# Performance work log

Hardware: AMD Instinct MI355X
Metric: run time of the kernel (lower is better)

## Reference

```python
import jax, jax.numpy as jnp
import numpy as np

WS = 7          # window size
NH = 16         # n_heads
DIM = 512
HEAD_DIM = DIM // NH
SCALE = HEAD_DIM ** -0.5


def _rel_pos_index(ws):
    coords = np.stack(np.meshgrid(np.arange(ws), np.arange(ws), indexing='ij'))  # [2,ws,ws]
    coords = coords.reshape(2, -1)                                               # [2,N]
    rel = coords[:, :, None] - coords[:, None, :]                                # [2,N,N]
    idx = (rel[0] + ws - 1) * (2 * ws - 1) + (rel[1] + ws - 1)                   # [N,N]
    return jnp.asarray(idx, dtype=jnp.int32)


def _window_partition(x, ws):
    B, H, W, C = x.shape
    x = x.reshape(B, H // ws, ws, W // ws, ws, C)
    x = x.transpose(0, 1, 3, 2, 4, 5)
    return x.reshape(-1, ws * ws, C)  # [B*nW, N, C]


def setup_inputs() -> dict:
    key = jax.random.key(0)
    k1, k2, k3 = jax.random.split(key, 3)
    qkv = jax.random.normal(k1, (3, 32, 56, 56, DIM), dtype=jnp.float32)
    mask = jax.random.normal(k2, (64, WS * WS, WS * WS), dtype=jnp.float32)
    bias_table = jax.random.normal(k3, ((2 * WS - 1) ** 2, NH), dtype=jnp.float32) * 0.02
    return {"qkv": qkv, "mask": mask, "bias_table": bias_table}


def reference(qkv, mask, bias_table):
    q, k, v = qkv[0], qkv[1], qkv[2]
    B, H, W, C = q.shape
    N = WS * WS
    # window partition + split heads -> [BS, NH, N, HEAD_DIM]
    def prep(x):
        x = _window_partition(x, WS)                       # [BS, N, C]
        BS = x.shape[0]
        return x.reshape(BS, N, NH, HEAD_DIM).transpose(0, 2, 1, 3)
    q, k, v = prep(q), prep(k), prep(v)
    BS = q.shape[0]

    attn = jnp.einsum('bhnd,bhmd->bhnm', q, k) * SCALE      # [BS, NH, N, N]

    idx = _rel_pos_index(WS)                                # [N, N] static
    rel_bias = bias_table[idx]                              # [N, N, NH]
    attn = attn + rel_bias.transpose(2, 0, 1)[None]         # [BS, NH, N, N]

    nW = mask.shape[0]
    attn = attn.reshape(BS // nW, nW, NH, N, N) + mask[None, :, None]
    attn = attn.reshape(BS, NH, N, N)

    attn = jax.nn.softmax(attn, axis=-1)
    x = jnp.einsum('bhnm,bhmd->bhnd', attn, v)              # [BS, NH, N, HEAD_DIM]
    return x.transpose(0, 2, 1, 3).reshape(BS, N, C)
```

## Files before the change

kernel.cpp:

```cpp
#include <hip/hip_runtime.h>

#define NTOK 49
#define NH 16
#define DIM 512
#define HD 32
#define HPB 4
#define SCALE 0.17677669529663687f

typedef __attribute__((ext_vector_type(8))) short short8;
typedef __attribute__((ext_vector_type(16))) float f32x16;

struct __attribute__((packed, aligned(4))) f4u { float x, y, z, w; };

__device__ __forceinline__ unsigned short f2b(float x) {
    union { float f; unsigned u; } v; v.f = x;
    unsigned u = v.u;
    u += 0x7fffu + ((u >> 16) & 1u);
    return (unsigned short)(u >> 16);
}

__device__ __forceinline__ float b2f(unsigned short b) {
    union { unsigned u; float f; } v; v.u = ((unsigned)b) << 16;
    return v.f;
}

__device__ __forceinline__ unsigned long long pack4(float4 v) {
    unsigned lo = (unsigned)f2b(v.x) | ((unsigned)f2b(v.y) << 16);
    unsigned hi = (unsigned)f2b(v.z) | ((unsigned)f2b(v.w) << 16);
    return (unsigned long long)lo | ((unsigned long long)hi << 32);
}

__device__ __forceinline__ short8 pack8s(float4 a, float4 b, float sc) {
    short8 r;
    r[0] = (short)f2b(a.x * sc); r[1] = (short)f2b(a.y * sc);
    r[2] = (short)f2b(a.z * sc); r[3] = (short)f2b(a.w * sc);
    r[4] = (short)f2b(b.x * sc); r[5] = (short)f2b(b.y * sc);
    r[6] = (short)f2b(b.z * sc); r[7] = (short)f2b(b.w * sc);
    return r;
}

__global__ __launch_bounds__(256, 4) void winattn_mfma(
    const float* __restrict__ qkv,
    const float* __restrict__ mask,
    const float* __restrict__ bias_table,
    float* __restrict__ out)
{
    __shared__ __align__(16) unsigned short Vr[HPB][64][32];
    __shared__ __align__(8)  unsigned short maskw[HPB][2404];
    __shared__ float biasw[HPB][176];
    __shared__ float invl[HPB][64];

    const int bx   = blockIdx.x;
    const int win  = bx >> 2;
    const int hg   = bx & 3;
    const int tid  = threadIdx.x;
    const int wave = tid >> 6;
    const int lane = tid & 63;
    const int ln   = lane & 31;
    const int h    = lane >> 5;
    const int head = hg * HPB + wave;

    const int b  = win >> 6;
    const int w  = win & 63;
    const int wr = w >> 3, wc = w & 7;

    const size_t plane = (size_t)32 * 56 * 56 * 512;
    const size_t wbase = (((size_t)(b * 56 + wr * 7)) * 56 + wc * 7) * 512 + head * HD;

    const int t0 = ln;
    const int t1 = (32 + ln <= 48) ? (32 + ln) : 48;
    float4 qv[2][4], kv[2][4];
    #pragma unroll
    for (int tt = 0; tt < 2; ++tt) {
        const int t  = tt ? t1 : t0;
        const int i  = t / 7, j = t - i * 7;
        const float* qp = qkv + wbase + (size_t)(i * 56 + j) * 512 + h * 8;
        const float* kp = qp + plane;
        qv[tt][0] = *(const float4*)(qp);
        qv[tt][1] = *(const float4*)(qp + 4);
        qv[tt][2] = *(const float4*)(qp + 16);
        qv[tt][3] = *(const float4*)(qp + 20);
        kv[tt][0] = *(const float4*)(kp);
        kv[tt][1] = *(const float4*)(kp + 4);
        kv[tt][2] = *(const float4*)(kp + 16);
        kv[tt][3] = *(const float4*)(kp + 20);
    }

    #pragma unroll
    for (int e = 0; e < 8; ++e) {
        const int idx = e * 64 + lane;
        const int t   = idx >> 3;
        const int d4  = idx & 7;
        unsigned long long vz = 0;
        if (t < NTOK) {
            const int i = t / 7, j = t - i * 7;
            vz = pack4(*(const float4*)(qkv + 2 * plane + wbase
                                        + (size_t)(i * 56 + j) * 512 + d4 * 4));
        }
        *(unsigned long long*)&Vr[wave][t][d4 * 4] = vz;
    }

    const float* mrow = mask + (size_t)w * 2401;
    for (int e = lane; e < 600; e += 64) {
        f4u mv = *(const f4u*)(mrow + 4 * e);
        unsigned long long pk =
              (unsigned long long)f2b(mv.x)
            | ((unsigned long long)f2b(mv.y) << 16)
            | ((unsigned long long)f2b(mv.z) << 32)
            | ((unsigned long long)f2b(mv.w) << 48);
        *(unsigned long long*)&maskw[wave][4 * e] = pk;
    }
    if (lane == 0) maskw[wave][2400] = f2b(mrow[2400]);

    for (int r = lane; r < 169; r += 64)
        biasw[wave][r] = bias_table[r * NH + head];

    short8 qfr[2][2], kfr[2][2];
    #pragma unroll
    for (int tt = 0; tt < 2; ++tt) {
        qfr[tt][0] = pack8s(qv[tt][0], qv[tt][1], SCALE);
        qfr[tt][1] = pack8s(qv[tt][2], qv[tt][3], SCALE);
        kfr[tt][0] = pack8s(kv[tt][0], kv[tt][1], 1.0f);
        kfr[tt][1] = pack8s(kv[tt][2], kv[tt][3], 1.0f);
    }

    f32x16 zer;
    #pragma unroll
    for (int i = 0; i < 16; ++i) zer[i] = 0.f;
    f32x16 acc[2][2];
    acc[0][0] = zer; acc[0][1] = zer; acc[1][0] = zer; acc[1][1] = zer;
    #pragma unroll
    for (int ks = 0; ks < 2; ++ks) {
        acc[0][0] = __builtin_amdgcn_mfma_f32_32x32x16_bf16(kfr[0][ks], qfr[0][ks], acc[0][0], 0, 0, 0);
        acc[0][1] = __builtin_amdgcn_mfma_f32_32x32x16_bf16(kfr[0][ks], qfr[1][ks], acc[0][1], 0, 0, 0);
        acc[1][0] = __builtin_amdgcn_mfma_f32_32x32x16_bf16(kfr[1][ks], qfr[0][ks], acc[1][0], 0, 0, 0);
        acc[1][1] = __builtin_amdgcn_mfma_f32_32x32x16_bf16(kfr[1][ks], qfr[1][ks], acc[1][1], 0, 0, 0);
    }

    unsigned wpk[2][2][8];
    #pragma unroll
    for (int nt = 0; nt < 2; ++nt) {
        const int n  = 32 * nt + ln;
        const int nc = n < NTOK ? n : NTOK - 1;
        const int i_n = nc / 7;
        const int tn  = nc + 6 * i_n + 84;
        float pl[2][16];
        float mx = -3.0e38f;
        #pragma unroll
        for (int mt = 0; mt < 2; ++mt) {
            #pragma unroll
            for (int r = 0; r < 16; ++r) {
                const int mb  = 32 * mt + (r & 3) + 8 * (r >> 2);
                const int m0  = mb, m1 = mb + 4;
                const int mc0 = m0 < NTOK ? m0 : NTOK - 1;
                const int mc1 = m1 < NTOK ? m1 : NTOK - 1;
                const int tm0 = mc0 + 6 * (mc0 / 7);
                const int tm1 = mc1 + 6 * (mc1 / 7);
                const int mc  = h ? mc1 : mc0;
                const int tm  = h ? tm1 : tm0;
                float s = acc[mt][nt][r] + biasw[wave][tn - tm]
                        + b2f(maskw[wave][nc * NTOK + mc]);
                const bool dead = h ? (m1 >= NTOK) : (m0 >= NTOK);
                s = dead ? -3.0e38f : s;
                pl[mt][r] = s;
                mx = fmaxf(mx, s);
            }
        }
        mx = fmaxf(mx, __shfl_xor(mx, 32));
        float sum = 0.f;
        #pragma unroll
        for (int mt = 0; mt < 2; ++mt) {
            #pragma unroll
            for (int g = 0; g < 8; ++g) {
                const int ia = (g < 4) ? g : g + 4;
                const float e0 = __expf(pl[mt][ia] - mx);
                const float e1 = __expf(pl[mt][ia + 4] - mx);
                sum += e0 + e1;
                wpk[nt][mt][g] = (unsigned)f2b(e0) | ((unsigned)f2b(e1) << 16);
            }
        }
        sum += __shfl_xor(sum, 32);
        if (h == 0 && n < NTOK)
            invl[wave][n] = 1.0f / sum;
    }

    f32x16 oacc[2];
    oacc[0] = zer; oacc[1] = zer;
    #pragma unroll
    for (int ksv = 0; ksv < 4; ++ksv) {
        short8 vf;
        #pragma unroll
        for (int j = 0; j < 8; ++j)
            vf[j] = (short)Vr[wave][16 * ksv + 8 * h + j][ln];
        const int mt = ksv >> 1;
        #pragma unroll
        for (int nt = 0; nt < 2; ++nt) {
            unsigned short alo[4], ahi[4];
            #pragma unroll
            for (int jj = 0; jj < 4; ++jj) {
                const unsigned W = wpk[nt][mt][(ksv & 1) * 4 + jj];
                const unsigned U = (unsigned)__shfl_xor((int)W, 32);
                alo[jj] = h ? (unsigned short)(U >> 16) : (unsigned short)(W & 0xffffu);
                ahi[jj] = h ? (unsigned short)(W >> 16) : (unsigned short)(U & 0xffffu);
            }
            short8 af;
            af[0] = (short)alo[0]; af[1] = (short)alo[1];
            af[2] = (short)alo[2]; af[3] = (short)alo[3];
            af[4] = (short)ahi[0]; af[5] = (short)ahi[1];
            af[6] = (short)ahi[2]; af[7] = (short)ahi[3];
            oacc[nt] = __builtin_amdgcn_mfma_f32_32x32x16_bf16(af, vf, oacc[nt], 0, 0, 0);
        }
    }

    const size_t obase = ((size_t)win * NTOK) * DIM + head * HD + ln;
    #pragma unroll
    for (int nt = 0; nt < 2; ++nt) {
        #pragma unroll
        for (int r = 0; r < 16; ++r) {
            const int nb = 32 * nt + (r & 3) + 8 * (r >> 2);
            const int n  = h ? nb + 4 : nb;
            if (n < NTOK)
                out[obase + (size_t)n * DIM] = oacc[nt][r] * invl[wave][n];
        }
    }
}

extern "C" void kernel_launch(void* const* d_in, const int* in_sizes, int n_in,
                              void* d_out, int out_size, void* d_ws, size_t ws_size,
                              hipStream_t stream) {
    const float* qkv        = (const float*)d_in[0];
    const float* mask       = (const float*)d_in[1];
    const float* bias_table = (const float*)d_in[2];
    float* out = (float*)d_out;

    const int nblocks = 2048 * (NH / HPB);
    winattn_mfma<<<nblocks, 256, 0, stream>>>(qkv, mask, bias_table, out);
}
```

Baseline: 197.4 us.

## Pre-expand bias per head, seed MFMA accumulators with mask+bias, load V directly

Adds a small pre-kernel that expands the relative-position bias table into a dense per-head 49x49 workspace. The main kernel drops all shared-memory staging of V, mask and bias. It loads mask plus bias straight from global memory into the QK MFMA accumulators and gathers V per lane into registers as bf16 fragments. This removes the LDS fill and bf16 mask conversion and the per-element index arithmetic in softmax. In exchange it issues more scattered global loads, uses more registers (occupancy hint lowered to 3), and adds a second launch.

```diff
diff --git a/kernel.cpp b/kernel.cpp
--- a/kernel.cpp
+++ b/kernel.cpp
@@ -4,30 +4,17 @@
 #define NH 16
 #define DIM 512
 #define HD 32
-#define HPB 4
 #define SCALE 0.17677669529663687f
+#define NEGINF -3.0e38f
 
 typedef __attribute__((ext_vector_type(8))) short short8;
 typedef __attribute__((ext_vector_type(16))) float f32x16;
-
-struct __attribute__((packed, aligned(4))) f4u { float x, y, z, w; };
 
 __device__ __forceinline__ unsigned short f2b(float x) {
     union { float f; unsigned u; } v; v.f = x;
     unsigned u = v.u;
     u += 0x7fffu + ((u >> 16) & 1u);
     return (unsigned short)(u >> 16);
-}
-
-__device__ __forceinline__ float b2f(unsigned short b) {
-    union { unsigned u; float f; } v; v.u = ((unsigned)b) << 16;
-    return v.f;
-}
-
-__device__ __forceinline__ unsigned long long pack4(float4 v) {
-    unsigned lo = (unsigned)f2b(v.x) | ((unsigned)f2b(v.y) << 16);
-    unsigned hi = (unsigned)f2b(v.z) | ((unsigned)f2b(v.w) << 16);
-    return (unsigned long long)lo | ((unsigned long long)hi << 32);
 }
 
 __device__ __forceinline__ short8 pack8s(float4 a, float4 b, float sc) {
@@ -39,16 +26,25 @@
     return r;
 }
 
-__global__ __launch_bounds__(256, 4) void winattn_mfma(
+__global__ __launch_bounds__(256) void bias_expand_kernel(
+    const float* __restrict__ bt, float* __restrict__ bexp)
+{
+    const int e = blockIdx.x * 256 + threadIdx.x;
+    if (e >= NH * NTOK * NTOK) return;
+    const int head = e / (NTOK * NTOK);
+    const int rem  = e % (NTOK * NTOK);
+    const int n = rem / NTOK, m = rem % NTOK;
+    const int rel = (n / 7 - m / 7 + 6) * 13 + (n % 7 - m % 7 + 6);
+    bexp[e] = bt[rel * NH + head];
+}
+
+__global__ __launch_bounds__(256, 3) void winattn_mfma(
     const float* __restrict__ qkv,
     const float* __restrict__ mask,
-    const float* __restrict__ bias_table,
+    const float* __restrict__ bexp,
     float* __restrict__ out)
 {
-    __shared__ __align__(16) unsigned short Vr[HPB][64][32];
-    __shared__ __align__(8)  unsigned short maskw[HPB][2404];
-    __shared__ float biasw[HPB][176];
-    __shared__ float invl[HPB][64];
+    __shared__ float invl[4][64];
 
     const int bx   = blockIdx.x;
     const int win  = bx >> 2;
@@ -58,7 +54,7 @@
     const int lane = tid & 63;
     const int ln   = lane & 31;
     const int h    = lane >> 5;
-    const int head = hg * HPB + wave;
+    const int head = hg * 4 + wave;
 
     const int b  = win >> 6;
     const int w  = win & 63;
@@ -86,34 +82,35 @@
         kv[tt][3] = *(const float4*)(kp + 20);
     }
 
-    #pragma unroll
-    for (int e = 0; e < 8; ++e) {
-        const int idx = e * 64 + lane;
-        const int t   = idx >> 3;
-        const int d4  = idx & 7;
-        unsigned long long vz = 0;
-        if (t < NTOK) {
-            const int i = t / 7, j = t - i * 7;
-            vz = pack4(*(const float4*)(qkv + 2 * plane + wbase
-                                        + (size_t)(i * 56 + j) * 512 + d4 * 4));
-        }
-        *(unsigned long long*)&Vr[wave][t][d4 * 4] = vz;
-    }
-
-    const float* mrow = mask + (size_t)w * 2401;
-    for (int e = lane; e < 600; e += 64) {
-        f4u mv = *(const f4u*)(mrow + 4 * e);
-        unsigned long long pk =
-              (unsigned long long)f2b(mv.x)
-            | ((unsigned long long)f2b(mv.y) << 16)
-            | ((unsigned long long)f2b(mv.z) << 32)
-            | ((unsigned long long)f2b(mv.w) << 48);
-        *(unsigned long long*)&maskw[wave][4 * e] = pk;
-    }
-    if (lane == 0) maskw[wave][2400] = f2b(mrow[2400]);
-
-    for (int r = lane; r < 169; r += 64)
-        biasw[wave][r] = bias_table[r * NH + head];
+    const float* mrow = mask + (size_t)w * (NTOK * NTOK);
+    const float* brow = bexp + (size_t)head * (NTOK * NTOK);
+    f32x16 acc[2][2];
+    #pragma unroll
+    for (int nt = 0; nt < 2; ++nt) {
+        const int n  = 32 * nt + ln;
+        const int nc = n < NTOK ? n : NTOK - 1;
+        const float* mh = mrow + nc * NTOK + h * 4;
+        const float* bh = brow + nc * NTOK + h * 4;
+        const float* m0 = mrow + nc * NTOK;
+        const float* b0 = brow + nc * NTOK;
+        #pragma unroll
+        for (int r = 0; r < 16; ++r) {
+            const int mb = (r & 3) + 8 * (r >> 2);
+            acc[0][nt][r] = mh[mb] + bh[mb];
+        }
+        #pragma unroll
+        for (int r = 0; r < 16; ++r) {
+            const int mb = 32 + (r & 3) + 8 * (r >> 2);
+            if (mb <= 43) {
+                acc[1][nt][r] = mh[mb] + bh[mb];
+            } else if (mb == 48) {
+                const float v = m0[48] + b0[48];
+                acc[1][nt][r] = h ? NEGINF : v;
+            } else {
+                acc[1][nt][r] = NEGINF;
+            }
+        }
+    }
 
     short8 qfr[2][2], kfr[2][2];
     #pragma unroll
@@ -124,11 +121,6 @@
         kfr[tt][1] = pack8s(kv[tt][2], kv[tt][3], 1.0f);
     }
 
-    f32x16 zer;
-    #pragma unroll
-    for (int i = 0; i < 16; ++i) zer[i] = 0.f;
-    f32x16 acc[2][2];
-    acc[0][0] = zer; acc[0][1] = zer; acc[1][0] = zer; acc[1][1] = zer;
     #pragma unroll
     for (int ks = 0; ks < 2; ++ks) {
         acc[0][0] = __builtin_amdgcn_mfma_f32_32x32x16_bf16(kfr[0][ks], qfr[0][ks], acc[0][0], 0, 0, 0);
@@ -137,35 +129,37 @@
         acc[1][1] = __builtin_amdgcn_mfma_f32_32x32x16_bf16(kfr[1][ks], qfr[1][ks], acc[1][1], 0, 0, 0);
     }
 
+    const float* vwin = qkv + 2 * plane + wbase;
+    short8 vfr[4];
+    #pragma unroll
+    for (int ksv = 0; ksv < 4; ++ksv) {
+        float vt[8];
+        #pragma unroll
+        for (int j = 0; j < 8; ++j) {
+            const int ta = 16 * ksv + j;
+            const int tb = 16 * ksv + 8 + j;
+            const int tac = ta < NTOK ? ta : NTOK - 1;
+            const int tbc = tb < NTOK ? tb : NTOK - 1;
+            const int offa = ((tac / 7) * 56 + tac % 7) * 512;
+            const int offb = ((tbc / 7) * 56 + tbc % 7) * 512;
+            vt[j] = vwin[(h ? offb : offa) + ln];
+        }
+        short8 vf;
+        #pragma unroll
+        for (int j = 0; j < 8; ++j) vf[j] = (short)f2b(vt[j]);
+        vfr[ksv] = vf;
+    }
+
     unsigned wpk[2][2][8];
     #pragma unroll
     for (int nt = 0; nt < 2; ++nt) {
-        const int n  = 32 * nt + ln;
-        const int nc = n < NTOK ? n : NTOK - 1;
-        const int i_n = nc / 7;
-        const int tn  = nc + 6 * i_n + 84;
-        float pl[2][16];
-        float mx = -3.0e38f;
-        #pragma unroll
-        for (int mt = 0; mt < 2; ++mt) {
+        const int n = 32 * nt + ln;
+        float mx = NEGINF;
+        #pragma unroll
+        for (int mt = 0; mt < 2; ++mt)
             #pragma unroll
-            for (int r = 0; r < 16; ++r) {
-                const int mb  = 32 * mt + (r & 3) + 8 * (r >> 2);
-                const int m0  = mb, m1 = mb + 4;
-                const int mc0 = m0 < NTOK ? m0 : NTOK - 1;
-                const int mc1 = m1 < NTOK ? m1 : NTOK - 1;
-                const int tm0 = mc0 + 6 * (mc0 / 7);
-                const int tm1 = mc1 + 6 * (mc1 / 7);
-                const int mc  = h ? mc1 : mc0;
-                const int tm  = h ? tm1 : tm0;
-                float s = acc[mt][nt][r] + biasw[wave][tn - tm]
-                        + b2f(maskw[wave][nc * NTOK + mc]);
-                const bool dead = h ? (m1 >= NTOK) : (m0 >= NTOK);
-                s = dead ? -3.0e38f : s;
-                pl[mt][r] = s;
-                mx = fmaxf(mx, s);
-            }
-        }
+            for (int r = 0; r < 16; ++r)
+                mx = fmaxf(mx, acc[mt][nt][r]);
         mx = fmaxf(mx, __shfl_xor(mx, 32));
         float sum = 0.f;
         #pragma unroll
@@ -173,8 +167,8 @@
             #pragma unroll
             for (int g = 0; g < 8; ++g) {
                 const int ia = (g < 4) ? g : g + 4;
-                const float e0 = __expf(pl[mt][ia] - mx);
-                const float e1 = __expf(pl[mt][ia + 4] - mx);
+                const float e0 = __expf(acc[mt][nt][ia] - mx);
+                const float e1 = __expf(acc[mt][nt][ia + 4] - mx);
                 sum += e0 + e1;
                 wpk[nt][mt][g] = (unsigned)f2b(e0) | ((unsigned)f2b(e1) << 16);
             }
@@ -185,13 +179,11 @@
     }
 
     f32x16 oacc[2];
-    oacc[0] = zer; oacc[1] = zer;
+    #pragma unroll
+    for (int i = 0; i < 16; ++i) { oacc[0][i] = 0.f; oacc[1][i] = 0.f; }
     #pragma unroll
     for (int ksv = 0; ksv < 4; ++ksv) {
-        short8 vf;
-        #pragma unroll
-        for (int j = 0; j < 8; ++j)
-            vf[j] = (short)Vr[wave][16 * ksv + 8 * h + j][ln];
+        const short8 vf = vfr[ksv];
         const int mt = ksv >> 1;
         #pragma unroll
         for (int nt = 0; nt < 2; ++nt) {
@@ -231,8 +223,9 @@
     const float* qkv        = (const float*)d_in[0];
     const float* mask       = (const float*)d_in[1];
     const float* bias_table = (const float*)d_in[2];
-    float* out = (float*)d_out;
-
-    const int nblocks = 2048 * (NH / HPB);
-    winattn_mfma<<<nblocks, 256, 0, stream>>>(qkv, mask, bias_table, out);
-}
+    float* out  = (float*)d_out;
+    float* bexp = (float*)d_ws;
+
+    bias_expand_kernel<<<(NH * NTOK * NTOK + 255) / 256, 256, 0, stream>>>(bias_table, bexp);
+    winattn_mfma<<<2048 * 4, 256, 0, stream>>>(qkv, mask, bexp, out);
+}
```

Measured after the change: 243.1 us. 1.23x slower.

## Share a precomputed mask-plus-bias tile per block and drop the softmax max pass

Applied to the files above, without the earlier changes.

A small pre-kernel expands the relative-position bias table into a dense per-head 49x49 fp32 bias in workspace. Blocks are remapped so one block handles a single (window, head) pair and its four waves cover four batch images. Those waves can then share one fp32 shared-memory tile of mask plus bias, instead of each wave loading its own bf16 mask copy and bias slice. The softmax no longer computes or subtracts a row max and instead exponentiates the logits directly. This cuts shared and L2 traffic and ALU work, but it adds a second launch and a __syncthreads. It also gives up overflow protection on large logits.

```diff
diff --git a/kernel.cpp b/kernel.cpp
--- a/kernel.cpp
+++ b/kernel.cpp
@@ -4,24 +4,17 @@
 #define NH 16
 #define DIM 512
 #define HD 32
-#define HPB 4
 #define SCALE 0.17677669529663687f
+#define NEGINF -3.0e38f
 
 typedef __attribute__((ext_vector_type(8))) short short8;
 typedef __attribute__((ext_vector_type(16))) float f32x16;
-
-struct __attribute__((packed, aligned(4))) f4u { float x, y, z, w; };
 
 __device__ __forceinline__ unsigned short f2b(float x) {
     union { float f; unsigned u; } v; v.f = x;
     unsigned u = v.u;
     u += 0x7fffu + ((u >> 16) & 1u);
     return (unsigned short)(u >> 16);
-}
-
-__device__ __forceinline__ float b2f(unsigned short b) {
-    union { unsigned u; float f; } v; v.u = ((unsigned)b) << 16;
-    return v.f;
 }
 
 __device__ __forceinline__ unsigned long long pack4(float4 v) {
@@ -39,33 +32,55 @@
     return r;
 }
 
+__global__ __launch_bounds__(256) void bias_expand_kernel(
+    const float* __restrict__ bt, float* __restrict__ bexp)
+{
+    const int e = blockIdx.x * 256 + threadIdx.x;
+    if (e >= NH * NTOK * NTOK) return;
+    const int head = e / (NTOK * NTOK);
+    const int rem  = e % (NTOK * NTOK);
+    const int n = rem / NTOK, m = rem % NTOK;
+    const int rel = (n / 7 - m / 7 + 6) * 13 + (n % 7 - m % 7 + 6);
+    bexp[e] = bt[rel * NH + head];
+}
+
 __global__ __launch_bounds__(256, 4) void winattn_mfma(
     const float* __restrict__ qkv,
     const float* __restrict__ mask,
-    const float* __restrict__ bias_table,
+    const float* __restrict__ bexp,
     float* __restrict__ out)
 {
-    __shared__ __align__(16) unsigned short Vr[HPB][64][32];
-    __shared__ __align__(8)  unsigned short maskw[HPB][2404];
-    __shared__ float biasw[HPB][176];
-    __shared__ float invl[HPB][64];
+    __shared__ float comb[NTOK][66];
+    __shared__ __align__(16) unsigned short Vr[4][64][32];
+    __shared__ float invl[4][64];
 
     const int bx   = blockIdx.x;
-    const int win  = bx >> 2;
-    const int hg   = bx & 3;
+    const int head = bx & 15;
+    const int w    = (bx >> 4) & 63;
+    const int bg   = bx >> 10;
     const int tid  = threadIdx.x;
     const int wave = tid >> 6;
     const int lane = tid & 63;
     const int ln   = lane & 31;
     const int h    = lane >> 5;
-    const int head = hg * HPB + wave;
-
-    const int b  = win >> 6;
-    const int w  = win & 63;
-    const int wr = w >> 3, wc = w & 7;
+    const int b    = bg * 4 + wave;
+    const int win  = b * 64 + w;
+    const int wr   = w >> 3, wc = w & 7;
 
     const size_t plane = (size_t)32 * 56 * 56 * 512;
     const size_t wbase = (((size_t)(b * 56 + wr * 7)) * 56 + wc * 7) * 512 + head * HD;
+
+    const float* mrow = mask + (size_t)w * (NTOK * NTOK);
+    const float* brow = bexp + (size_t)head * (NTOK * NTOK);
+    for (int e = tid; e < NTOK * 64; e += 256) {
+        const int n = e >> 6, m = e & 63;
+        float v = NEGINF;
+        if (m < NTOK) {
+            const int o = n * NTOK + m;
+            v = mrow[o] + brow[o];
+        }
+        comb[n][m] = v;
+    }
 
     const int t0 = ln;
     const int t1 = (32 + ln <= 48) ? (32 + ln) : 48;
@@ -100,20 +115,7 @@
         *(unsigned long long*)&Vr[wave][t][d4 * 4] = vz;
     }
 
-    const float* mrow = mask + (size_t)w * 2401;
-    for (int e = lane; e < 600; e += 64) {
-        f4u mv = *(const f4u*)(mrow + 4 * e);
-        unsigned long long pk =
-              (unsigned long long)f2b(mv.x)
-            | ((unsigned long long)f2b(mv.y) << 16)
-            | ((unsigned long long)f2b(mv.z) << 32)
-            | ((unsigned long long)f2b(mv.w) << 48);
-        *(unsigned long long*)&maskw[wave][4 * e] = pk;
-    }
-    if (lane == 0) maskw[wave][2400] = f2b(mrow[2400]);
-
-    for (int r = lane; r < 169; r += 64)
-        biasw[wave][r] = bias_table[r * NH + head];
+    __syncthreads();
 
     short8 qfr[2][2], kfr[2][2];
     #pragma unroll
@@ -142,39 +144,16 @@
     for (int nt = 0; nt < 2; ++nt) {
         const int n  = 32 * nt + ln;
         const int nc = n < NTOK ? n : NTOK - 1;
-        const int i_n = nc / 7;
-        const int tn  = nc + 6 * i_n + 84;
-        float pl[2][16];
-        float mx = -3.0e38f;
-        #pragma unroll
-        for (int mt = 0; mt < 2; ++mt) {
-            #pragma unroll
-            for (int r = 0; r < 16; ++r) {
-                const int mb  = 32 * mt + (r & 3) + 8 * (r >> 2);
-                const int m0  = mb, m1 = mb + 4;
-                const int mc0 = m0 < NTOK ? m0 : NTOK - 1;
-                const int mc1 = m1 < NTOK ? m1 : NTOK - 1;
-                const int tm0 = mc0 + 6 * (mc0 / 7);
-                const int tm1 = mc1 + 6 * (mc1 / 7);
-                const int mc  = h ? mc1 : mc0;
-                const int tm  = h ? tm1 : tm0;
-                float s = acc[mt][nt][r] + biasw[wave][tn - tm]
-                        + b2f(maskw[wave][nc * NTOK + mc]);
-                const bool dead = h ? (m1 >= NTOK) : (m0 >= NTOK);
-                s = dead ? -3.0e38f : s;
-                pl[mt][r] = s;
-                mx = fmaxf(mx, s);
-            }
-        }
-        mx = fmaxf(mx, __shfl_xor(mx, 32));
+        const float* crow = &comb[nc][4 * h];
         float sum = 0.f;
         #pragma unroll
         for (int mt = 0; mt < 2; ++mt) {
             #pragma unroll
             for (int g = 0; g < 8; ++g) {
                 const int ia = (g < 4) ? g : g + 4;
-                const float e0 = __expf(pl[mt][ia] - mx);
-                const float e1 = __expf(pl[mt][ia + 4] - mx);
+                const int mb = (ia & 3) + 8 * (ia >> 2) + 32 * mt;
+                const float e0 = __expf(acc[mt][nt][ia]     + crow[mb]);
+                const float e1 = __expf(acc[mt][nt][ia + 4] + crow[mb + 8]);
                 sum += e0 + e1;
                 wpk[nt][mt][g] = (unsigned)f2b(e0) | ((unsigned)f2b(e1) << 16);
             }
@@ -231,8 +210,9 @@
     const float* qkv        = (const float*)d_in[0];
     const float* mask       = (const float*)d_in[1];
     const float* bias_table = (const float*)d_in[2];
-    float* out = (float*)d_out;
-
-    const int nblocks = 2048 * (NH / HPB);
-    winattn_mfma<<<nblocks, 256, 0, stream>>>(qkv, mask, bias_table, out);
-}
+    float* out  = (float*)d_out;
+    float* bexp = (float*)d_ws;
+
+    bias_expand_kernel<<<(NH * NTOK * NTOK + 255) / 256, 256, 0, stream>>>(bias_table, bexp);
+    winattn_mfma<<<8192, 256, 0, stream>>>(qkv, mask, bexp, out);
+}
```

Measured after the change: 218.6 us. 10.8% more time.
